# Kernel optimization log

Hardware: AMD Instinct MI355X
Metric: run time of the kernel (lower is better)

The kernel has to match this reference:

```python
import jax, jax.numpy as jnp
import numpy as np

TEMPERATURE = 0.1
BASE_TEMPERATURE = 0.07
N = 8192
D = 128


def setup_inputs() -> dict:
    key = jax.random.key(0)
    kf, kl = jax.random.split(key)
    feats = jax.random.normal(kf, (N, 1, D), dtype=jnp.float32)
    # contrastive embeddings are typically L2-normalized upstream
    feats = feats / jnp.linalg.norm(feats, axis=-1, keepdims=True)
    labels = jax.random.randint(kl, (N,), 0, 2, dtype=jnp.int32)
    return {"feats": feats, "labels": labels}


def reference(feats, labels):
    # feats: [anchor_num, n_view=1, D]; labels: [anchor_num] binary fg/bg
    anchor_num, n_view, d = feats.shape
    n = anchor_num * n_view  # n_view == 1 in this module
    contrast_feature = feats.reshape(n, d)

    lab = labels.reshape(-1, 1)
    pos_mask = (lab == lab.T).astype(feats.dtype)  # [N, N]
    neg_mask = 1.0 - pos_mask

    # [N, N] similarity logits
    logits = jnp.matmul(contrast_feature, contrast_feature.T) / TEMPERATURE
    logits_max = jax.lax.stop_gradient(jnp.max(logits, axis=1, keepdims=True))
    logits = logits - logits_max

    # mask out self-contrast on the diagonal (logits_mask in torch code)
    idx = jnp.arange(n)
    pos_mask = pos_mask.at[idx, idx].set(0.0)

    exp_logits = jnp.exp(logits)
    neg_logits = jnp.sum(exp_logits * neg_mask, axis=1, keepdims=True)  # [N,1]
    log_prob = logits - jnp.log(exp_logits + neg_logits)

    mean_log_prob_pos = jnp.sum(pos_mask * log_prob, axis=1) / jnp.sum(pos_mask, axis=1)
    loss = -(TEMPERATURE / BASE_TEMPERATURE) * mean_log_prob_pos
    return jnp.mean(loss)
```

## Files before the change

kernel.cpp:

```cpp
#include <hip/hip_runtime.h>
#include <hip/hip_bf16.h>

#define NN 8192
#define DD 128

typedef short bf16x8 __attribute__((ext_vector_type(8)));
typedef float f32x4 __attribute__((ext_vector_type(4)));

#define LOG2E 1.4426950408889634f
#define K2f   14.426950408889634f

#define M_OFF    (NN * DD * 2)
#define LABF_OFF (M_OFF + NN * 4)
#define G_OFF    (LABF_OFF + NN * 4)
#define CNT_OFF  (G_OFF + 256 * 4)
#define EG_OFF   (CNT_OFF + 256)
#define ELG_OFF  (EG_OFF + NN * 4)

#define BROWS 256
#define BCOLS 512
#define ITERS (BCOLS / 16)

__device__ __forceinline__ unsigned short f2bf(float x) {
    unsigned u = __float_as_uint(x);
    u = (u + 0x7FFFu + ((u >> 16) & 1u)) >> 16;
    return (unsigned short)u;
}

__global__ __launch_bounds__(256) void prep_kernel(const float* __restrict__ F,
        const int* __restrict__ labels, unsigned short* __restrict__ F16,
        float* __restrict__ M, float* __restrict__ labf, float* __restrict__ G,
        int* __restrict__ cnt1, float* __restrict__ Eg, float* __restrict__ Elg) {
    __shared__ float sG[256];
    __shared__ int scnt;
    const int tid = threadIdx.x;
    sG[tid] = 0.f;
    if (tid == 0) scnt = 0;
    __syncthreads();
    const int wave = tid >> 6, lane = tid & 63;
    const int half = lane >> 5, l32 = lane & 31;
    const int rb = blockIdx.x * 32;
    if (tid < 32) { Eg[rb + tid] = 0.f; Elg[rb + tid] = 0.f; }
    int mycnt = 0;
    float g1a[4] = {0.f, 0.f, 0.f, 0.f}, gta[4] = {0.f, 0.f, 0.f, 0.f};
    #pragma unroll
    for (int it = 0; it < 4; ++it) {
        const int row = rb + it * 8 + wave * 2 + half;
        const int lab = labels[row];
        const float lf = (float)lab;
        const float4 f = *reinterpret_cast<const float4*>(F + row * DD + l32 * 4);
        ushort4 u;
        u.x = f2bf(f.x); u.y = f2bf(f.y); u.z = f2bf(f.z); u.w = f2bf(f.w);
        *reinterpret_cast<ushort4*>(F16 + row * DD + l32 * 4) = u;
        g1a[0] = fmaf(lf, f.x, g1a[0]); gta[0] += f.x;
        g1a[1] = fmaf(lf, f.y, g1a[1]); gta[1] += f.y;
        g1a[2] = fmaf(lf, f.z, g1a[2]); gta[2] += f.z;
        g1a[3] = fmaf(lf, f.w, g1a[3]); gta[3] += f.w;
        float ss = fmaf(f.x, f.x, fmaf(f.y, f.y, fmaf(f.z, f.z, f.w * f.w)));
        #pragma unroll
        for (int off = 1; off < 32; off <<= 1) ss += __shfl_xor(ss, off);
        if (l32 == 0) {
            M[row] = 10.0f * ss;
            labf[row] = lf;
            mycnt += lab;
        }
    }
    #pragma unroll
    for (int j = 0; j < 4; ++j) {
        atomicAdd(&sG[l32 * 4 + j], g1a[j]);
        atomicAdd(&sG[128 + l32 * 4 + j], gta[j]);
    }
    if (l32 == 0 && mycnt) atomicAdd(&scnt, mycnt);
    __syncthreads();
    atomicAdd(&G[tid], sG[tid]);
    if (tid == 0) atomicAdd(cnt1, scnt);
}

__global__ __launch_bounds__(512, 4) void loss_kernel(
        const unsigned short* __restrict__ F16, const float* __restrict__ M,
        const float* __restrict__ labf, float* __restrict__ Eg,
        float* __restrict__ Elg) {
    __shared__ unsigned short Bt[2][2048];
    __shared__ float Lab[BCOLS];
    const int tid  = threadIdx.x;
    const int wave = tid >> 6, lane = tid & 63;
    const int quad = lane >> 4, l16 = lane & 15;
    const int rb = (blockIdx.x & 31) * BROWS;
    const int cb = (blockIdx.x >> 5) * BCOLS;

    Lab[tid] = labf[cb + tid];

    const int rw = rb + wave * 32;
    bf16x8 a[2][4];
    #pragma unroll
    for (int m = 0; m < 2; m++)
        #pragma unroll
        for (int kb = 0; kb < 4; kb++)
            a[m][kb] = *reinterpret_cast<const bf16x8*>(
                F16 + (rw + m * 16 + l16) * DD + kb * 32 + quad * 8);

    float mneg[2][4];
    #pragma unroll
    for (int m = 0; m < 2; m++)
        #pragma unroll
        for (int r = 0; r < 4; r++)
            mneg[m][r] = -M[rw + m * 16 + quad * 4 + r] * LOG2E;

    {
        const int c = lane & 15, q = lane >> 4;
        if (wave == 0) {
            const unsigned short* src = F16 + (cb + q) * DD + c * 8;
            #pragma unroll
            for (int i = 0; i < 4; i++) {
                const bf16x8 v = *reinterpret_cast<const bf16x8*>(src + i * 4 * DD);
                const int col = i * 4 + q;
                *reinterpret_cast<bf16x8*>(&Bt[0][c * 128 + ((col ^ c) & 15) * 8]) = v;
            }
        }
    }
    float accE[2][4] = {}, accEl[2][4] = {};
    __syncthreads();

    for (int it = 0; it < ITERS; ++it) {
        const int cur = it & 1;
        const bool stager = (wave == ((it + 1) & 7)) && (it + 1 < ITERS);
        bf16x8 v[4];
        const int c = lane & 15, q = lane >> 4;
        if (stager) {
            const unsigned short* src = F16 + (cb + (it + 1) * 16 + q) * DD + c * 8;
            #pragma unroll
            for (int i = 0; i < 4; i++)
                v[i] = *reinterpret_cast<const bf16x8*>(src + i * 4 * DD);
        }

        bf16x8 bfr[4];
        #pragma unroll
        for (int kb = 0; kb < 4; kb++) {
            const int cr = kb * 4 + quad;
            bfr[kb] = *reinterpret_cast<const bf16x8*>(
                &Bt[cur][cr * 128 + ((l16 ^ cr) & 15) * 8]);
        }
        const float lc = Lab[it * 16 + l16];

        f32x4 d0 = {0.f, 0.f, 0.f, 0.f}, d1 = {0.f, 0.f, 0.f, 0.f};
        #pragma unroll
        for (int kb = 0; kb < 4; kb++) {
            d0 = __builtin_amdgcn_mfma_f32_16x16x32_bf16(a[0][kb], bfr[kb], d0, 0, 0, 0);
            d1 = __builtin_amdgcn_mfma_f32_16x16x32_bf16(a[1][kb], bfr[kb], d1, 0, 0, 0);
        }

        #pragma unroll
        for (int m = 0; m < 2; m++) {
            #pragma unroll
            for (int r = 0; r < 4; r++) {
                const float vv = (m == 0) ? d0[r] : d1[r];
                const float e = exp2f(fmaf(vv, K2f, mneg[m][r]));
                accE[m][r] += e;
                accEl[m][r] = fmaf(lc, e, accEl[m][r]);
            }
        }

        if (stager) {
            unsigned short* dst = &Bt[cur ^ 1][0];
            #pragma unroll
            for (int i = 0; i < 4; i++) {
                const int col = i * 4 + q;
                *reinterpret_cast<bf16x8*>(dst + c * 128 + ((col ^ c) & 15) * 8) = v[i];
            }
        }
        __syncthreads();
    }

    #pragma unroll
    for (int m = 0; m < 2; m++) {
        #pragma unroll
        for (int r = 0; r < 4; r++) {
            float e = accE[m][r], el = accEl[m][r];
            #pragma unroll
            for (int off = 1; off < 16; off <<= 1) {
                e  += __shfl_xor(e,  off);
                el += __shfl_xor(el, off);
            }
            if (l16 == 0) {
                const int row = rw + m * 16 + quad * 4 + r;
                atomicAdd(&Eg[row], e);
                atomicAdd(&Elg[row], el);
            }
        }
    }
}

__global__ __launch_bounds__(256) void final_kernel(
        const unsigned short* __restrict__ F16, const float* __restrict__ M,
        const int* __restrict__ labels, const float* __restrict__ G,
        const int* __restrict__ cnt1, const float* __restrict__ Eg,
        const float* __restrict__ Elg, float* __restrict__ out) {
    __shared__ float sG[256];
    __shared__ float wsum[4];
    const int tid = threadIdx.x;
    sG[tid] = G[tid];
    __syncthreads();
    const int row = blockIdx.x * 256 + tid;
    const int lr = labels[row];
    float dot = 0.f;
    const unsigned short* f = F16 + row * DD;
    #pragma unroll
    for (int k = 0; k < DD; k += 8) {
        const bf16x8 fv = *reinterpret_cast<const bf16x8*>(f + k);
        #pragma unroll
        for (int j = 0; j < 8; j++) {
            const float fj = __uint_as_float(((unsigned)(unsigned short)fv[j]) << 16);
            const float g1 = sG[k + j];
            const float gl = lr ? g1 : (sG[128 + k + j] - g1);
            dot = fmaf(fj, gl, dot);
        }
    }
    const float E    = Eg[row];
    const float El   = Elg[row];
    const float Epos = lr ? El : (E - El);
    const float Si   = E - Epos;
    const float mi   = M[row];
    const int   c1   = *cnt1;
    const float cntp1 = (float)(lr ? c1 : (NN - c1));
    const float cnt   = cntp1 - 1.f;
    const float sum_l   = fmaf(10.f, dot, -cntp1 * mi);
    const float sum_log = cntp1 * __logf(Si) + Epos / Si;
    float li = -(10.f / 7.f) * (sum_l - sum_log) / cnt;
    #pragma unroll
    for (int off = 1; off < 64; off <<= 1) li += __shfl_xor(li, off);
    if ((tid & 63) == 0) wsum[tid >> 6] = li;
    __syncthreads();
    if (tid == 0)
        atomicAdd(out, (wsum[0] + wsum[1] + wsum[2] + wsum[3]) * (1.0f / NN));
}

extern "C" void kernel_launch(void* const* d_in, const int* in_sizes, int n_in,
                              void* d_out, int out_size, void* d_ws, size_t ws_size,
                              hipStream_t stream) {
    const float* F      = (const float*)d_in[0];
    const int*   labels = (const int*)d_in[1];
    float*       out    = (float*)d_out;
    char*        ws     = (char*)d_ws;
    unsigned short* F16 = (unsigned short*)ws;
    float*       M      = (float*)(ws + M_OFF);
    float*       labf   = (float*)(ws + LABF_OFF);
    float*       G      = (float*)(ws + G_OFF);
    int*         cnt1   = (int*)(ws + CNT_OFF);
    float*       Eg     = (float*)(ws + EG_OFF);
    float*       Elg    = (float*)(ws + ELG_OFF);

    hipMemsetAsync(out, 0, sizeof(float), stream);
    hipMemsetAsync(ws + G_OFF, 0, 256 * 4 + 256, stream);

    prep_kernel<<<NN / 32, 256, 0, stream>>>(F, labels, F16, M, labf, G, cnt1, Eg, Elg);
    loss_kernel<<<512, 512, 0, stream>>>(F16, M, labf, Eg, Elg);
    final_kernel<<<NN / 256, 256, 0, stream>>>(F16, M, labels, G, cnt1, Eg, Elg, out);
}
```

Baseline: 109.4 us.

## Widen LDS column tile to 32 and spread staging across all threads

The per-iteration B tile grows from 16 to 32 columns, so the loop runs half as many iterations and needs half as many block barriers. Staging of the next tile is no longer done by one rotating wave loading four vectors; every thread now loads one 16-byte vector and writes it to the other LDS buffer after compute. The swizzle widens to 5 bits to match the new tile width. The final iteration issues a redundant wraparound load, and the doubled LDS footprint could affect occupancy.

```diff
diff --git a/kernel.cpp b/kernel.cpp
--- a/kernel.cpp
+++ b/kernel.cpp
@@ -19,7 +19,8 @@
 
 #define BROWS 256
 #define BCOLS 512
-#define ITERS (BCOLS / 16)
+#define TCOLS 32
+#define ITERS (BCOLS / TCOLS)
 
 __device__ __forceinline__ unsigned short f2bf(float x) {
     unsigned u = __float_as_uint(x);
@@ -80,7 +81,7 @@
         const unsigned short* __restrict__ F16, const float* __restrict__ M,
         const float* __restrict__ labf, float* __restrict__ Eg,
         float* __restrict__ Elg) {
-    __shared__ unsigned short Bt[2][2048];
+    __shared__ unsigned short Bt[2][TCOLS * DD];
     __shared__ float Lab[BCOLS];
     const int tid  = threadIdx.x;
     const int wave = tid >> 6, lane = tid & 63;
@@ -106,68 +107,52 @@
         for (int r = 0; r < 4; r++)
             mneg[m][r] = -M[rw + m * 16 + quad * 4 + r] * LOG2E;
 
-    {
-        const int c = lane & 15, q = lane >> 4;
-        if (wave == 0) {
-            const unsigned short* src = F16 + (cb + q) * DD + c * 8;
-            #pragma unroll
-            for (int i = 0; i < 4; i++) {
-                const bf16x8 v = *reinterpret_cast<const bf16x8*>(src + i * 4 * DD);
-                const int col = i * 4 + q;
-                *reinterpret_cast<bf16x8*>(&Bt[0][c * 128 + ((col ^ c) & 15) * 8]) = v;
-            }
-        }
-    }
+    const int scol = tid >> 4;
+    const int sc   = tid & 15;
+    const unsigned short* sbase = F16 + (cb + scol) * DD + sc * 8;
+    const int sdst = sc * (TCOLS * 8) + (((scol ^ sc) & 31) * 8);
+
+    *reinterpret_cast<bf16x8*>(&Bt[0][sdst]) =
+        *reinterpret_cast<const bf16x8*>(sbase);
+
     float accE[2][4] = {}, accEl[2][4] = {};
     __syncthreads();
 
     for (int it = 0; it < ITERS; ++it) {
         const int cur = it & 1;
-        const bool stager = (wave == ((it + 1) & 7)) && (it + 1 < ITERS);
-        bf16x8 v[4];
-        const int c = lane & 15, q = lane >> 4;
-        if (stager) {
-            const unsigned short* src = F16 + (cb + (it + 1) * 16 + q) * DD + c * 8;
-            #pragma unroll
-            for (int i = 0; i < 4; i++)
-                v[i] = *reinterpret_cast<const bf16x8*>(src + i * 4 * DD);
-        }
-
-        bf16x8 bfr[4];
-        #pragma unroll
-        for (int kb = 0; kb < 4; kb++) {
-            const int cr = kb * 4 + quad;
-            bfr[kb] = *reinterpret_cast<const bf16x8*>(
-                &Bt[cur][cr * 128 + ((l16 ^ cr) & 15) * 8]);
-        }
-        const float lc = Lab[it * 16 + l16];
-
-        f32x4 d0 = {0.f, 0.f, 0.f, 0.f}, d1 = {0.f, 0.f, 0.f, 0.f};
-        #pragma unroll
-        for (int kb = 0; kb < 4; kb++) {
-            d0 = __builtin_amdgcn_mfma_f32_16x16x32_bf16(a[0][kb], bfr[kb], d0, 0, 0, 0);
-            d1 = __builtin_amdgcn_mfma_f32_16x16x32_bf16(a[1][kb], bfr[kb], d1, 0, 0, 0);
-        }
-
-        #pragma unroll
-        for (int m = 0; m < 2; m++) {
-            #pragma unroll
-            for (int r = 0; r < 4; r++) {
-                const float vv = (m == 0) ? d0[r] : d1[r];
-                const float e = exp2f(fmaf(vv, K2f, mneg[m][r]));
-                accE[m][r] += e;
-                accEl[m][r] = fmaf(lc, e, accEl[m][r]);
-            }
-        }
-
-        if (stager) {
-            unsigned short* dst = &Bt[cur ^ 1][0];
-            #pragma unroll
-            for (int i = 0; i < 4; i++) {
-                const int col = i * 4 + q;
-                *reinterpret_cast<bf16x8*>(dst + c * 128 + ((col ^ c) & 15) * 8) = v[i];
-            }
-        }
+        const int itn = (it + 1) & (ITERS - 1);
+        const bf16x8 vn = *reinterpret_cast<const bf16x8*>(sbase + itn * TCOLS * DD);
+
+        #pragma unroll
+        for (int g = 0; g < 2; ++g) {
+            bf16x8 bfr[4];
+            #pragma unroll
+            for (int kb = 0; kb < 4; kb++) {
+                const int cr = kb * 4 + quad;
+                const int col = g * 16 + l16;
+                bfr[kb] = *reinterpret_cast<const bf16x8*>(
+                    &Bt[cur][cr * (TCOLS * 8) + (((col ^ cr) & 31) * 8)]);
+            }
+            f32x4 d0 = {0.f, 0.f, 0.f, 0.f}, d1 = {0.f, 0.f, 0.f, 0.f};
+            #pragma unroll
+            for (int kb = 0; kb < 4; kb++) {
+                d0 = __builtin_amdgcn_mfma_f32_16x16x32_bf16(a[0][kb], bfr[kb], d0, 0, 0, 0);
+                d1 = __builtin_amdgcn_mfma_f32_16x16x32_bf16(a[1][kb], bfr[kb], d1, 0, 0, 0);
+            }
+            const float lc = Lab[it * TCOLS + g * 16 + l16];
+            #pragma unroll
+            for (int m = 0; m < 2; m++) {
+                #pragma unroll
+                for (int r = 0; r < 4; r++) {
+                    const float vv = (m == 0) ? d0[r] : d1[r];
+                    const float e = exp2f(fmaf(vv, K2f, mneg[m][r]));
+                    accE[m][r] += e;
+                    accEl[m][r] = fmaf(lc, e, accEl[m][r]);
+                }
+            }
+        }
+
+        *reinterpret_cast<bf16x8*>(&Bt[cur ^ 1][sdst]) = vn;
         __syncthreads();
     }
 
```

Result: faster. 106.5 us (-2.6%).
